# Performance work log

Hardware: AMD Instinct MI355X
Metric: run time of the kernel (lower is better)

The kernel has to match this reference:

```python
import jax, jax.numpy as jnp
import numpy as np

NU, NV = 8192, 8192
IN_DIM, HID, NCLS = 128, 64, 5


def setup_inputs() -> dict:
    key = jax.random.key(0)
    k1, k2, k3, k4, k5, k6, k7 = jax.random.split(key, 7)
    return {
        "u": jax.random.normal(k1, (NU, IN_DIM), dtype=jnp.float32),
        "v": jax.random.normal(k2, (NV, IN_DIM), dtype=jnp.float32),
        "adj": jax.random.uniform(k3, (NU, NV), dtype=jnp.float32),
        "degree": jax.random.uniform(k4, (NU + NV,), dtype=jnp.float32),
        "u_weight": jax.random.normal(k5, (NCLS, IN_DIM, HID), dtype=jnp.float32),
        "v_weight": jax.random.normal(k6, (NCLS, IN_DIM, HID), dtype=jnp.float32),
        "bias": jax.random.normal(k7, (HID,), dtype=jnp.float32),
        "r": 4,
    }


def reference(u, v, adj, degree, u_weight, v_weight, bias, r):
    # Sum weight slices for rating classes 0..r (r is a static Python int).
    Wu = jnp.sum(u_weight[: r + 1], axis=0)  # [IN_DIM, HID]
    Wv = jnp.sum(v_weight[: r + 1], axis=0)
    # Dropout is identity at p=0.0 (eval mode).
    su = u @ Wu  # [NU, HID]
    sv = v @ Wv  # [NV, HID]
    nu = adj.shape[0]
    # Block adjacency [[0, A], [A^T, 0]] row-scaled by diag(degree), applied to
    # concat(su, sv) -- computed block-wise, same math without the dense block matrix.
    top = degree[:nu, None] * (adj @ sv)      # [NU, HID]
    bot = degree[nu:, None] * (adj.T @ su)    # [NV, HID]
    return jnp.concatenate([top, bot], axis=0) + bias
```

## Files before the change

### kernel.cpp

```cpp
#include <hip/hip_runtime.h>
#include <stdint.h>


#define HID 64
#define IN_DIM 128
#define NROWS 8192
#define NCLS 5

typedef float f32x4 __attribute__((ext_vector_type(4)));
typedef short s16x8 __attribute__((ext_vector_type(8)));
typedef unsigned short u16;

#define PACK_SIDE 524288

static __device__ __forceinline__ short f2b(float x) {
    unsigned u = __builtin_bit_cast(unsigned, x);
    return (short)((u + 0x7FFFu + ((u >> 16) & 1u)) >> 16);
}

__global__ __launch_bounds__(256, 2) void k_prep(
    const float* __restrict__ u, const float* __restrict__ v,
    const float* __restrict__ uw, const float* __restrict__ vw,
    const int* __restrict__ rp, u16* __restrict__ ws)
{
    __shared__ float W[IN_DIM * HID];
    __shared__ float X[64 * 129];

    const int y = blockIdx.y;
    const float* __restrict__ src  = y ? v  : u;
    const float* __restrict__ wsrc = y ? vw : uw;
    u16* __restrict__ dstP = ws + (size_t)y * PACK_SIDE;
    const int i0 = blockIdx.x * 64;
    const int t = threadIdx.x;
    int r = *rp; if (r > NCLS - 1) r = NCLS - 1; if (r < 0) r = 0;

    for (int idx = t; idx < IN_DIM * HID; idx += 256) {
        float s = 0.f;
        for (int c = 0; c <= r; ++c) s += wsrc[c * (IN_DIM * HID) + idx];
        W[idx] = s;
    }
    #pragma unroll
    for (int qq = 0; qq < 8; ++qq) {
        int idx = t + qq * 256;
        int row = idx >> 5, c4 = idx & 31;
        f32x4 val = *(const f32x4*)&src[(size_t)(i0 + row) * IN_DIM + c4 * 4];
        float* d = &X[row * 129 + c4 * 4];
        d[0] = val[0]; d[1] = val[1]; d[2] = val[2]; d[3] = val[3];
    }
    __syncthreads();

    const int i = t & 63, h0 = (t >> 6) * 16;
    float acc[16];
    #pragma unroll
    for (int k = 0; k < 16; ++k) acc[k] = 0.f;
    for (int c = 0; c < IN_DIM; ++c) {
        float uv = X[i * 129 + c];
        const f32x4* wr = (const f32x4*)&W[c * HID + h0];
        f32x4 w0 = wr[0], w1 = wr[1], w2 = wr[2], w3 = wr[3];
        acc[0]  += uv * w0[0]; acc[1]  += uv * w0[1];
        acc[2]  += uv * w0[2]; acc[3]  += uv * w0[3];
        acc[4]  += uv * w1[0]; acc[5]  += uv * w1[1];
        acc[6]  += uv * w1[2]; acc[7]  += uv * w1[3];
        acc[8]  += uv * w2[0]; acc[9]  += uv * w2[1];
        acc[10] += uv * w2[2]; acc[11] += uv * w2[3];
        acc[12] += uv * w3[0]; acc[13] += uv * w3[1];
        acc[14] += uv * w3[2]; acc[15] += uv * w3[3];
    }
    const int iL = i0 + i;
    u16* __restrict__ dp = dstP
        + (((size_t)(iL >> 5) * 4 + (h0 >> 4)) << 9)
        + ((iL >> 3) & 3) * 128
        + (iL & 7);
    #pragma unroll
    for (int hh = 0; hh < 16; ++hh)
        dp[hh * 8] = (u16)f2b(acc[hh]);
}

__global__ __launch_bounds__(256, 2) void k_main(
    const float* __restrict__ adj, const float* __restrict__ degree,
    const float* __restrict__ bias, const u16* __restrict__ ws,
    float* __restrict__ out)
{
    __shared__ float S[4][64 * 33];

    const int mode = blockIdx.y;
    const int bx = blockIdx.x;
    const int t = threadIdx.x;
    const int w = t >> 6, l = t & 63;
    const int q = l >> 4, l15 = l & 15;
    const int m0 = bx * 32;
    const unsigned a = (unsigned)(bx >> 1);
    const int kbase = w * 2048;
    const u16* __restrict__ BP = ws + (mode == 0 ? (size_t)PACK_SIDE : 0);
    const u16* __restrict__ BPl = BP + (size_t)l * 8;

    f32x4 acc[2][4];
    #pragma unroll
    for (int i = 0; i < 2; ++i)
        #pragma unroll
        for (int j = 0; j < 4; ++j) acc[i][j] = (f32x4){0.f, 0.f, 0.f, 0.f};

    if (mode == 0) {
        const float* __restrict__ ap0 = adj + (size_t)(m0 + l15) * NROWS;
        const float* __restrict__ ap1 = ap0 + (size_t)16 * NROWS;
        for (int tau = 0; tau < 32; ++tau) {
            const int k0 = kbase + (int)(((a + tau) & 31u) << 6);
            #pragma unroll
            for (int kh = 0; kh < 2; ++kh) {
                const int k = k0 + kh * 32 + q * 8;
                const int kb = (k0 >> 5) + kh;
                f32x4 a00 = *(const f32x4*)(ap0 + k);
                f32x4 a01 = *(const f32x4*)(ap0 + k + 4);
                f32x4 a10 = *(const f32x4*)(ap1 + k);
                f32x4 a11 = *(const f32x4*)(ap1 + k + 4);
                s16x8 bf[4];
                #pragma unroll
                for (int nn = 0; nn < 4; ++nn)
                    bf[nn] = *(const s16x8*)(BPl + ((size_t)(kb * 4 + nn) << 9));
                s16x8 af0, af1;
                af0[0]=f2b(a00[0]); af0[1]=f2b(a00[1]); af0[2]=f2b(a00[2]); af0[3]=f2b(a00[3]);
                af0[4]=f2b(a01[0]); af0[5]=f2b(a01[1]); af0[6]=f2b(a01[2]); af0[7]=f2b(a01[3]);
                af1[0]=f2b(a10[0]); af1[1]=f2b(a10[1]); af1[2]=f2b(a10[2]); af1[3]=f2b(a10[3]);
                af1[4]=f2b(a11[0]); af1[5]=f2b(a11[1]); af1[6]=f2b(a11[2]); af1[7]=f2b(a11[3]);
                #pragma unroll
                for (int nn = 0; nn < 4; ++nn) {
                    acc[0][nn] = __builtin_amdgcn_mfma_f32_16x16x32_bf16(af0, bf[nn], acc[0][nn], 0, 0, 0);
                    acc[1][nn] = __builtin_amdgcn_mfma_f32_16x16x32_bf16(af1, bf[nn], acc[1][nn], 0, 0, 0);
                }
            }
        }
    } else {
        float* __restrict__ T = S[w];
        const int wr_r = l >> 3;
        const int wr_c = (l & 7) * 4;
        const float* __restrict__ cb = adj + m0 + wr_c;
        for (int tau = 0; tau < 32; ++tau) {
            const int i0 = kbase + (int)(((a - tau) & 31u) << 6);
            f32x4 tr[8];
            #pragma unroll
            for (int c = 0; c < 8; ++c)
                tr[c] = *(const f32x4*)(cb + (size_t)(i0 + c * 8 + wr_r) * NROWS);
            #pragma unroll
            for (int c = 0; c < 8; ++c) {
                float* d = &T[(c * 8 + wr_r) * 33 + wr_c];
                d[0] = tr[c][0]; d[1] = tr[c][1]; d[2] = tr[c][2]; d[3] = tr[c][3];
            }
            asm volatile("s_waitcnt lgkmcnt(0)" ::: "memory");
            #pragma unroll
            for (int kh = 0; kh < 2; ++kh) {
                const int kb = (i0 >> 5) + kh;
                s16x8 bf[4];
                #pragma unroll
                for (int nn = 0; nn < 4; ++nn)
                    bf[nn] = *(const s16x8*)(BPl + ((size_t)(kb * 4 + nn) << 9));
                s16x8 af[2];
                #pragma unroll
                for (int mt = 0; mt < 2; ++mt) {
                    const int j = mt * 16 + l15;
                    #pragma unroll
                    for (int tt = 0; tt < 8; ++tt)
                        af[mt][tt] = f2b(T[(kh * 32 + q * 8 + tt) * 33 + j]);
                }
                #pragma unroll
                for (int nn = 0; nn < 4; ++nn) {
                    acc[0][nn] = __builtin_amdgcn_mfma_f32_16x16x32_bf16(af[0], bf[nn], acc[0][nn], 0, 0, 0);
                    acc[1][nn] = __builtin_amdgcn_mfma_f32_16x16x32_bf16(af[1], bf[nn], acc[1][nn], 0, 0, 0);
                }
            }
            asm volatile("" ::: "memory");
        }
    }

    asm volatile("" ::: "memory");
    {
        float* __restrict__ P = S[w];
        #pragma unroll
        for (int mt = 0; mt < 2; ++mt)
            #pragma unroll
            for (int nn = 0; nn < 4; ++nn)
                #pragma unroll
                for (int rg = 0; rg < 4; ++rg)
                    P[(mt * 16 + q * 4 + rg) * 64 + nn * 16 + l15] = acc[mt][nn][rg];
    }
    __syncthreads();

    const int e0 = t * 8;
    const int m = e0 >> 6, n = e0 & 63;
    f32x4 s0 = (f32x4){0.f,0.f,0.f,0.f}, s1 = s0;
    #pragma unroll
    for (int ww = 0; ww < 4; ++ww) {
        s0 += *(const f32x4*)&S[ww][e0];
        s1 += *(const f32x4*)&S[ww][e0 + 4];
    }
    const int grow = (mode ? NROWS : 0) + m0 + m;
    const float d = degree[grow];
    f32x4 b0 = *(const f32x4*)&bias[n];
    f32x4 b1 = *(const f32x4*)&bias[n + 4];
    f32x4 o0 = d * s0 + b0;
    f32x4 o1 = d * s1 + b1;
    *(f32x4*)&out[(size_t)grow * HID + n]     = o0;
    *(f32x4*)&out[(size_t)grow * HID + n + 4] = o1;
}

extern "C" void kernel_launch(void* const* d_in, const int* in_sizes, int n_in,
                              void* d_out, int out_size, void* d_ws, size_t ws_size,
                              hipStream_t stream) {
    (void)in_sizes; (void)n_in; (void)out_size; (void)ws_size;
    const float* u      = (const float*)d_in[0];
    const float* v      = (const float*)d_in[1];
    const float* adj    = (const float*)d_in[2];
    const float* degree = (const float*)d_in[3];
    const float* uw     = (const float*)d_in[4];
    const float* vw     = (const float*)d_in[5];
    const float* bias   = (const float*)d_in[6];
    const int*   rp     = (const int*)d_in[7];
    u16*   ws  = (u16*)d_ws;
    float* out = (float*)d_out;

    k_prep<<<dim3(128, 2), 256, 0, stream>>>(u, v, uw, vw, rp, ws);
    k_main<<<dim3(256, 2), 256, 0, stream>>>(adj, degree, bias, ws, out);
}
```

Before: 467.4 us.

## Prefetch next adjacency tile in registers and rebalance mode-0 blocks

Both branches of the main kernel now load the next adjacency tile into registers while the current tile is converted and fed to MFMA, software-pipelining global loads against compute. Mode-0 blocks shrink to 16 rows, giving 512 such blocks, and the grid is flattened to 768 blocks with launch bounds raised to 3 waves per SIMD for more occupancy. The double-buffered registers raise register pressure. Since the adjacency matrix is read twice, halving mode-0 tile height may lower reuse of the packed B operand.

```diff
diff --git a/kernel.cpp b/kernel.cpp
--- a/kernel.cpp
+++ b/kernel.cpp
@@ -76,79 +76,135 @@
         dp[hh * 8] = (u16)f2b(acc[hh]);
 }
 
-__global__ __launch_bounds__(256, 2) void k_main(
+__global__ __launch_bounds__(256, 3) void k_main(
     const float* __restrict__ adj, const float* __restrict__ degree,
     const float* __restrict__ bias, const u16* __restrict__ ws,
     float* __restrict__ out)
 {
     __shared__ float S[4][64 * 33];
 
-    const int mode = blockIdx.y;
-    const int bx = blockIdx.x;
+    const int bxr = blockIdx.x;
+    const int mode = (bxr >= 512);
     const int t = threadIdx.x;
     const int w = t >> 6, l = t & 63;
     const int q = l >> 4, l15 = l & 15;
-    const int m0 = bx * 32;
-    const unsigned a = (unsigned)(bx >> 1);
     const int kbase = w * 2048;
     const u16* __restrict__ BP = ws + (mode == 0 ? (size_t)PACK_SIDE : 0);
     const u16* __restrict__ BPl = BP + (size_t)l * 8;
 
-    f32x4 acc[2][4];
-    #pragma unroll
-    for (int i = 0; i < 2; ++i)
-        #pragma unroll
-        for (int j = 0; j < 4; ++j) acc[i][j] = (f32x4){0.f, 0.f, 0.f, 0.f};
-
     if (mode == 0) {
-        const float* __restrict__ ap0 = adj + (size_t)(m0 + l15) * NROWS;
-        const float* __restrict__ ap1 = ap0 + (size_t)16 * NROWS;
-        for (int tau = 0; tau < 32; ++tau) {
-            const int k0 = kbase + (int)(((a + tau) & 31u) << 6);
-            #pragma unroll
-            for (int kh = 0; kh < 2; ++kh) {
-                const int k = k0 + kh * 32 + q * 8;
-                const int kb = (k0 >> 5) + kh;
-                f32x4 a00 = *(const f32x4*)(ap0 + k);
-                f32x4 a01 = *(const f32x4*)(ap0 + k + 4);
-                f32x4 a10 = *(const f32x4*)(ap1 + k);
-                f32x4 a11 = *(const f32x4*)(ap1 + k + 4);
-                s16x8 bf[4];
-                #pragma unroll
-                for (int nn = 0; nn < 4; ++nn)
-                    bf[nn] = *(const s16x8*)(BPl + ((size_t)(kb * 4 + nn) << 9));
-                s16x8 af0, af1;
-                af0[0]=f2b(a00[0]); af0[1]=f2b(a00[1]); af0[2]=f2b(a00[2]); af0[3]=f2b(a00[3]);
-                af0[4]=f2b(a01[0]); af0[5]=f2b(a01[1]); af0[6]=f2b(a01[2]); af0[7]=f2b(a01[3]);
-                af1[0]=f2b(a10[0]); af1[1]=f2b(a10[1]); af1[2]=f2b(a10[2]); af1[3]=f2b(a10[3]);
-                af1[4]=f2b(a11[0]); af1[5]=f2b(a11[1]); af1[6]=f2b(a11[2]); af1[7]=f2b(a11[3]);
-                #pragma unroll
-                for (int nn = 0; nn < 4; ++nn) {
-                    acc[0][nn] = __builtin_amdgcn_mfma_f32_16x16x32_bf16(af0, bf[nn], acc[0][nn], 0, 0, 0);
-                    acc[1][nn] = __builtin_amdgcn_mfma_f32_16x16x32_bf16(af1, bf[nn], acc[1][nn], 0, 0, 0);
+        const int bx = bxr;
+        const int m0 = bx * 16;
+        const unsigned a = (unsigned)(bx >> 2);
+        const float* __restrict__ ap0 = adj + (size_t)(m0 + l15) * NROWS + q * 8;
+
+        f32x4 acc[4];
+        #pragma unroll
+        for (int nn = 0; nn < 4; ++nn) acc[nn] = (f32x4){0.f, 0.f, 0.f, 0.f};
+
+        {
+            const int k0 = kbase + (int)((a & 31u) << 6);
+            f32x4 c00 = *(const f32x4*)(ap0 + k0);
+            f32x4 c01 = *(const f32x4*)(ap0 + k0 + 4);
+            f32x4 c10 = *(const f32x4*)(ap0 + k0 + 32);
+            f32x4 c11 = *(const f32x4*)(ap0 + k0 + 36);
+            for (int tau = 0; tau < 32; ++tau) {
+                const int k0c = kbase + (int)(((a + tau) & 31u) << 6);
+                const int tnx = (tau < 31) ? tau + 1 : tau;
+                const int k0n = kbase + (int)(((a + tnx) & 31u) << 6);
+                f32x4 n00 = *(const f32x4*)(ap0 + k0n);
+                f32x4 n01 = *(const f32x4*)(ap0 + k0n + 4);
+                f32x4 n10 = *(const f32x4*)(ap0 + k0n + 32);
+                f32x4 n11 = *(const f32x4*)(ap0 + k0n + 36);
+
+                #pragma unroll
+                for (int kh = 0; kh < 2; ++kh) {
+                    const int kb = (k0c >> 5) + kh;
+                    s16x8 bf[4];
+                    #pragma unroll
+                    for (int nn = 0; nn < 4; ++nn)
+                        bf[nn] = *(const s16x8*)(BPl + ((size_t)(kb * 4 + nn) << 9));
+                    s16x8 af;
+                    if (kh == 0) {
+                        af[0]=f2b(c00[0]); af[1]=f2b(c00[1]); af[2]=f2b(c00[2]); af[3]=f2b(c00[3]);
+                        af[4]=f2b(c01[0]); af[5]=f2b(c01[1]); af[6]=f2b(c01[2]); af[7]=f2b(c01[3]);
+                    } else {
+                        af[0]=f2b(c10[0]); af[1]=f2b(c10[1]); af[2]=f2b(c10[2]); af[3]=f2b(c10[3]);
+                        af[4]=f2b(c11[0]); af[5]=f2b(c11[1]); af[6]=f2b(c11[2]); af[7]=f2b(c11[3]);
+                    }
+                    #pragma unroll
+                    for (int nn = 0; nn < 4; ++nn)
+                        acc[nn] = __builtin_amdgcn_mfma_f32_16x16x32_bf16(af, bf[nn], acc[nn], 0, 0, 0);
                 }
+                c00 = n00; c01 = n01; c10 = n10; c11 = n11;
             }
         }
-    } else {
+
+        asm volatile("" ::: "memory");
+        {
+            float* __restrict__ P = S[w];
+            #pragma unroll
+            for (int nn = 0; nn < 4; ++nn)
+                #pragma unroll
+                for (int rg = 0; rg < 4; ++rg)
+                    P[(q * 4 + rg) * 64 + nn * 16 + l15] = acc[nn][rg];
+        }
+        __syncthreads();
+
+        const int e0 = t * 4;
+        const int m = e0 >> 6, n = e0 & 63;
+        f32x4 s = (f32x4){0.f, 0.f, 0.f, 0.f};
+        #pragma unroll
+        for (int ww = 0; ww < 4; ++ww) s += *(const f32x4*)&S[ww][e0];
+        const int grow = m0 + m;
+        const float d = degree[grow];
+        f32x4 b = *(const f32x4*)&bias[n];
+        *(f32x4*)&out[(size_t)grow * HID + n] = d * s + b;
+        return;
+    }
+
+    {
+        const int bx = bxr - 512;
+        const int m0 = bx * 32;
+        const unsigned a = (unsigned)(bx >> 1);
         float* __restrict__ T = S[w];
         const int wr_r = l >> 3;
         const int wr_c = (l & 7) * 4;
         const float* __restrict__ cb = adj + m0 + wr_c;
-        for (int tau = 0; tau < 32; ++tau) {
-            const int i0 = kbase + (int)(((a - tau) & 31u) << 6);
-            f32x4 tr[8];
+
+        f32x4 acc[2][4];
+        #pragma unroll
+        for (int i = 0; i < 2; ++i)
+            #pragma unroll
+            for (int j = 0; j < 4; ++j) acc[i][j] = (f32x4){0.f, 0.f, 0.f, 0.f};
+
+        f32x4 tr[8];
+        {
+            const int i0 = kbase + (int)((a & 31u) << 6);
             #pragma unroll
             for (int c = 0; c < 8; ++c)
                 tr[c] = *(const f32x4*)(cb + (size_t)(i0 + c * 8 + wr_r) * NROWS);
+        }
+        for (int tau = 0; tau < 32; ++tau) {
+            const int i0c = kbase + (int)(((a - tau) & 31u) << 6);
+            const int tnx = (tau < 31) ? tau + 1 : tau;
+            const int i0n = kbase + (int)(((a - tnx) & 31u) << 6);
+
             #pragma unroll
             for (int c = 0; c < 8; ++c) {
                 float* d = &T[(c * 8 + wr_r) * 33 + wr_c];
                 d[0] = tr[c][0]; d[1] = tr[c][1]; d[2] = tr[c][2]; d[3] = tr[c][3];
             }
             asm volatile("s_waitcnt lgkmcnt(0)" ::: "memory");
+
+            f32x4 trn[8];
+            #pragma unroll
+            for (int c = 0; c < 8; ++c)
+                trn[c] = *(const f32x4*)(cb + (size_t)(i0n + c * 8 + wr_r) * NROWS);
+
             #pragma unroll
             for (int kh = 0; kh < 2; ++kh) {
-                const int kb = (i0 >> 5) + kh;
+                const int kb = (i0c >> 5) + kh;
                 s16x8 bf[4];
                 #pragma unroll
                 for (int nn = 0; nn < 4; ++nn)
@@ -168,38 +224,38 @@
                 }
             }
             asm volatile("" ::: "memory");
-        }
-    }
-
-    asm volatile("" ::: "memory");
-    {
-        float* __restrict__ P = S[w];
-        #pragma unroll
-        for (int mt = 0; mt < 2; ++mt)
-            #pragma unroll
-            for (int nn = 0; nn < 4; ++nn)
-                #pragma unroll
-                for (int rg = 0; rg < 4; ++rg)
-                    P[(mt * 16 + q * 4 + rg) * 64 + nn * 16 + l15] = acc[mt][nn][rg];
-    }
-    __syncthreads();
-
-    const int e0 = t * 8;
-    const int m = e0 >> 6, n = e0 & 63;
-    f32x4 s0 = (f32x4){0.f,0.f,0.f,0.f}, s1 = s0;
-    #pragma unroll
-    for (int ww = 0; ww < 4; ++ww) {
-        s0 += *(const f32x4*)&S[ww][e0];
-        s1 += *(const f32x4*)&S[ww][e0 + 4];
-    }
-    const int grow = (mode ? NROWS : 0) + m0 + m;
-    const float d = degree[grow];
-    f32x4 b0 = *(const f32x4*)&bias[n];
-    f32x4 b1 = *(const f32x4*)&bias[n + 4];
-    f32x4 o0 = d * s0 + b0;
-    f32x4 o1 = d * s1 + b1;
-    *(f32x4*)&out[(size_t)grow * HID + n]     = o0;
-    *(f32x4*)&out[(size_t)grow * HID + n + 4] = o1;
+            #pragma unroll
+            for (int c = 0; c < 8; ++c) tr[c] = trn[c];
+        }
+
+        asm volatile("" ::: "memory");
+        {
+            float* __restrict__ P = S[w];
+            #pragma unroll
+            for (int mt = 0; mt < 2; ++mt)
+                #pragma unroll
+                for (int nn = 0; nn < 4; ++nn)
+                    #pragma unroll
+                    for (int rg = 0; rg < 4; ++rg)
+                        P[(mt * 16 + q * 4 + rg) * 64 + nn * 16 + l15] = acc[mt][nn][rg];
+        }
+        __syncthreads();
+
+        const int e0 = t * 8;
+        const int m = e0 >> 6, n = e0 & 63;
+        f32x4 s0 = (f32x4){0.f,0.f,0.f,0.f}, s1 = s0;
+        #pragma unroll
+        for (int ww = 0; ww < 4; ++ww) {
+            s0 += *(const f32x4*)&S[ww][e0];
+            s1 += *(const f32x4*)&S[ww][e0 + 4];
+        }
+        const int grow = NROWS + m0 + m;
+        const float d = degree[grow];
+        f32x4 b0 = *(const f32x4*)&bias[n];
+        f32x4 b1 = *(const f32x4*)&bias[n + 4];
+        *(f32x4*)&out[(size_t)grow * HID + n]     = d * s0 + b0;
+        *(f32x4*)&out[(size_t)grow * HID + n + 4] = d * s1 + b1;
+    }
 }
 
 extern "C" void kernel_launch(void* const* d_in, const int* in_sizes, int n_in,
@@ -218,5 +274,5 @@
     float* out = (float*)d_out;
 
     k_prep<<<dim3(128, 2), 256, 0, stream>>>(u, v, uw, vw, rp, ws);
-    k_main<<<dim3(256, 2), 256, 0, stream>>>(adj, degree, bias, ws, out);
-}
+    k_main<<<dim3(768),    256, 0, stream>>>(adj, degree, bias, ws, out);
+}
```

Measured after the change: 489.4 us. 1.05x slower.

## Read adjacency once per 256x256 tile for both products, reduce partials in separate kernel

Applied to the files above, without the earlier changes.

Replaces the two-mode main kernel, which streamed adj once row-wise and once transposed, with a single pass. Each block loads a 256x256 adj tile into swizzled bf16 LDS, and its waves compute both the adj@sv and adj^T@su contributions from that tile. Per-tile partial sums go to large fp32 workspace buffers (32 partials per output row). A new finalize kernel then sums those partials and applies degree and bias. This removes the second adj read and the strided transposed loads, but adds roughly 134MB of partial-sum writes and reads plus an extra launch. It also relies on a much larger workspace, and the transposed side builds its fragments from scalar 16-bit LDS reads.

```diff
diff --git a/kernel.cpp b/kernel.cpp
--- a/kernel.cpp
+++ b/kernel.cpp
@@ -9,6 +9,7 @@
 
 typedef float f32x4 __attribute__((ext_vector_type(4)));
 typedef short s16x8 __attribute__((ext_vector_type(8)));
+typedef short s16x4 __attribute__((ext_vector_type(4)));
 typedef unsigned short u16;
 
 #define PACK_SIDE 524288
@@ -77,129 +78,142 @@
 }
 
 __global__ __launch_bounds__(256, 2) void k_main(
-    const float* __restrict__ adj, const float* __restrict__ degree,
-    const float* __restrict__ bias, const u16* __restrict__ ws,
-    float* __restrict__ out)
+    const float* __restrict__ adj, const u16* __restrict__ ws,
+    float* __restrict__ wst, float* __restrict__ wsb)
 {
-    __shared__ float S[4][64 * 33];
-
-    const int mode = blockIdx.y;
+    __shared__ u16 P[64][256];
+
     const int bx = blockIdx.x;
+    const int R0 = (bx >> 5) * 256, C0 = (bx & 31) * 256;
     const int t = threadIdx.x;
     const int w = t >> 6, l = t & 63;
     const int q = l >> 4, l15 = l & 15;
-    const int m0 = bx * 32;
-    const unsigned a = (unsigned)(bx >> 1);
-    const int kbase = w * 2048;
-    const u16* __restrict__ BP = ws + (mode == 0 ? (size_t)PACK_SIDE : 0);
-    const u16* __restrict__ BPl = BP + (size_t)l * 8;
-
-    f32x4 acc[2][4];
-    #pragma unroll
-    for (int i = 0; i < 2; ++i)
+    const u16* __restrict__ BPl_u = ws + (size_t)l * 8;
+    const u16* __restrict__ BPl_v = ws + PACK_SIDE + (size_t)l * 8;
+
+    f32x4 accB[8][4];
+    #pragma unroll
+    for (int mt = 0; mt < 8; ++mt)
         #pragma unroll
-        for (int j = 0; j < 4; ++j) acc[i][j] = (f32x4){0.f, 0.f, 0.f, 0.f};
-
-    if (mode == 0) {
-        const float* __restrict__ ap0 = adj + (size_t)(m0 + l15) * NROWS;
-        const float* __restrict__ ap1 = ap0 + (size_t)16 * NROWS;
-        for (int tau = 0; tau < 32; ++tau) {
-            const int k0 = kbase + (int)(((a + tau) & 31u) << 6);
-            #pragma unroll
-            for (int kh = 0; kh < 2; ++kh) {
-                const int k = k0 + kh * 32 + q * 8;
-                const int kb = (k0 >> 5) + kh;
-                f32x4 a00 = *(const f32x4*)(ap0 + k);
-                f32x4 a01 = *(const f32x4*)(ap0 + k + 4);
-                f32x4 a10 = *(const f32x4*)(ap1 + k);
-                f32x4 a11 = *(const f32x4*)(ap1 + k + 4);
-                s16x8 bf[4];
-                #pragma unroll
-                for (int nn = 0; nn < 4; ++nn)
-                    bf[nn] = *(const s16x8*)(BPl + ((size_t)(kb * 4 + nn) << 9));
-                s16x8 af0, af1;
-                af0[0]=f2b(a00[0]); af0[1]=f2b(a00[1]); af0[2]=f2b(a00[2]); af0[3]=f2b(a00[3]);
-                af0[4]=f2b(a01[0]); af0[5]=f2b(a01[1]); af0[6]=f2b(a01[2]); af0[7]=f2b(a01[3]);
-                af1[0]=f2b(a10[0]); af1[1]=f2b(a10[1]); af1[2]=f2b(a10[2]); af1[3]=f2b(a10[3]);
-                af1[4]=f2b(a11[0]); af1[5]=f2b(a11[1]); af1[6]=f2b(a11[2]); af1[7]=f2b(a11[3]);
-                #pragma unroll
-                for (int nn = 0; nn < 4; ++nn) {
-                    acc[0][nn] = __builtin_amdgcn_mfma_f32_16x16x32_bf16(af0, bf[nn], acc[0][nn], 0, 0, 0);
-                    acc[1][nn] = __builtin_amdgcn_mfma_f32_16x16x32_bf16(af1, bf[nn], acc[1][nn], 0, 0, 0);
+        for (int nn = 0; nn < 4; ++nn) accB[mt][nn] = (f32x4){0.f, 0.f, 0.f, 0.f};
+
+    for (int p = 0; p < 4; ++p) {
+        {
+            const float* __restrict__ src =
+                adj + (size_t)(R0 + p * 64 + w * 16) * NROWS + C0 + l * 4;
+            #pragma unroll
+            for (int rr = 0; rr < 16; rr += 4) {
+                f32x4 d0 = *(const f32x4*)(src + (size_t)(rr + 0) * NROWS);
+                f32x4 d1 = *(const f32x4*)(src + (size_t)(rr + 1) * NROWS);
+                f32x4 d2 = *(const f32x4*)(src + (size_t)(rr + 2) * NROWS);
+                f32x4 d3 = *(const f32x4*)(src + (size_t)(rr + 3) * NROWS);
+                #pragma unroll
+                for (int i = 0; i < 4; ++i) {
+                    f32x4 d = (i == 0) ? d0 : (i == 1) ? d1 : (i == 2) ? d2 : d3;
+                    const int row = w * 16 + rr + i;
+                    s16x4 b;
+                    b[0] = f2b(d[0]); b[1] = f2b(d[1]);
+                    b[2] = f2b(d[2]); b[3] = f2b(d[3]);
+                    *(s16x4*)&P[row][(((l >> 1) ^ (row & 7)) << 3) + ((l & 1) << 2)] = b;
                 }
             }
         }
-    } else {
-        float* __restrict__ T = S[w];
-        const int wr_r = l >> 3;
-        const int wr_c = (l & 7) * 4;
-        const float* __restrict__ cb = adj + m0 + wr_c;
-        for (int tau = 0; tau < 32; ++tau) {
-            const int i0 = kbase + (int)(((a - tau) & 31u) << 6);
-            f32x4 tr[8];
-            #pragma unroll
-            for (int c = 0; c < 8; ++c)
-                tr[c] = *(const f32x4*)(cb + (size_t)(i0 + c * 8 + wr_r) * NROWS);
-            #pragma unroll
-            for (int c = 0; c < 8; ++c) {
-                float* d = &T[(c * 8 + wr_r) * 33 + wr_c];
-                d[0] = tr[c][0]; d[1] = tr[c][1]; d[2] = tr[c][2]; d[3] = tr[c][3];
-            }
-            asm volatile("s_waitcnt lgkmcnt(0)" ::: "memory");
-            #pragma unroll
-            for (int kh = 0; kh < 2; ++kh) {
-                const int kb = (i0 >> 5) + kh;
+        __syncthreads();
+
+        if (w < 2) {
+            f32x4 accT[2][4];
+            #pragma unroll
+            for (int mt = 0; mt < 2; ++mt)
+                #pragma unroll
+                for (int nn = 0; nn < 4; ++nn) accT[mt][nn] = (f32x4){0.f, 0.f, 0.f, 0.f};
+            #pragma unroll
+            for (int kk = 0; kk < 8; ++kk) {
+                const int kb = (C0 >> 5) + kk;
                 s16x8 bf[4];
                 #pragma unroll
                 for (int nn = 0; nn < 4; ++nn)
-                    bf[nn] = *(const s16x8*)(BPl + ((size_t)(kb * 4 + nn) << 9));
-                s16x8 af[2];
+                    bf[nn] = *(const s16x8*)(BPl_v + ((size_t)(kb * 4 + nn) << 9));
                 #pragma unroll
                 for (int mt = 0; mt < 2; ++mt) {
-                    const int j = mt * 16 + l15;
-                    #pragma unroll
-                    for (int tt = 0; tt < 8; ++tt)
-                        af[mt][tt] = f2b(T[(kh * 32 + q * 8 + tt) * 33 + j]);
-                }
-                #pragma unroll
-                for (int nn = 0; nn < 4; ++nn) {
-                    acc[0][nn] = __builtin_amdgcn_mfma_f32_16x16x32_bf16(af[0], bf[nn], acc[0][nn], 0, 0, 0);
-                    acc[1][nn] = __builtin_amdgcn_mfma_f32_16x16x32_bf16(af[1], bf[nn], acc[1][nn], 0, 0, 0);
+                    const int row = w * 32 + mt * 16 + l15;
+                    s16x8 af = *(const s16x8*)&P[row][((kk * 4 + q) ^ (row & 7)) << 3];
+                    #pragma unroll
+                    for (int nn = 0; nn < 4; ++nn)
+                        accT[mt][nn] = __builtin_amdgcn_mfma_f32_16x16x32_bf16(
+                            af, bf[nn], accT[mt][nn], 0, 0, 0);
                 }
             }
-            asm volatile("" ::: "memory");
+            float* __restrict__ WT = wst + (size_t)(bx & 31) * (NROWS * HID)
+                                   + (size_t)(R0 + p * 64 + w * 32) * HID;
+            #pragma unroll
+            for (int mt = 0; mt < 2; ++mt)
+                #pragma unroll
+                for (int nn = 0; nn < 4; ++nn)
+                    #pragma unroll
+                    for (int rg = 0; rg < 4; ++rg)
+                        WT[(size_t)(mt * 16 + q * 4 + rg) * HID + nn * 16 + l15] =
+                            accT[mt][nn][rg];
+        } else {
+            #pragma unroll
+            for (int kk = 0; kk < 2; ++kk) {
+                const int kb = (R0 >> 5) + p * 2 + kk;
+                s16x8 bf[4];
+                #pragma unroll
+                for (int nn = 0; nn < 4; ++nn)
+                    bf[nn] = *(const s16x8*)(BPl_u + ((size_t)(kb * 4 + nn) << 9));
+                #pragma unroll
+                for (int mt = 0; mt < 8; ++mt) {
+                    const int j = (w - 2) * 128 + mt * 16 + l15;
+                    s16x8 af;
+                    #pragma unroll
+                    for (int tt = 0; tt < 8; ++tt) {
+                        const int row = kk * 32 + q * 8 + tt;
+                        af[tt] = (short)P[row][(((j >> 3) ^ tt) << 3) + (j & 7)];
+                    }
+                    #pragma unroll
+                    for (int nn = 0; nn < 4; ++nn)
+                        accB[mt][nn] = __builtin_amdgcn_mfma_f32_16x16x32_bf16(
+                            af, bf[nn], accB[mt][nn], 0, 0, 0);
+                }
+            }
         }
-    }
-
-    asm volatile("" ::: "memory");
-    {
-        float* __restrict__ P = S[w];
+        __syncthreads();
+    }
+
+    if (w >= 2) {
+        float* __restrict__ WB = wsb + (size_t)(bx >> 5) * (NROWS * HID)
+                               + (size_t)(C0 + (w - 2) * 128) * HID;
         #pragma unroll
-        for (int mt = 0; mt < 2; ++mt)
+        for (int mt = 0; mt < 8; ++mt)
             #pragma unroll
             for (int nn = 0; nn < 4; ++nn)
                 #pragma unroll
                 for (int rg = 0; rg < 4; ++rg)
-                    P[(mt * 16 + q * 4 + rg) * 64 + nn * 16 + l15] = acc[mt][nn][rg];
-    }
-    __syncthreads();
-
-    const int e0 = t * 8;
-    const int m = e0 >> 6, n = e0 & 63;
-    f32x4 s0 = (f32x4){0.f,0.f,0.f,0.f}, s1 = s0;
-    #pragma unroll
-    for (int ww = 0; ww < 4; ++ww) {
-        s0 += *(const f32x4*)&S[ww][e0];
-        s1 += *(const f32x4*)&S[ww][e0 + 4];
-    }
-    const int grow = (mode ? NROWS : 0) + m0 + m;
+                    WB[(size_t)(mt * 16 + q * 4 + rg) * HID + nn * 16 + l15] =
+                        accB[mt][nn][rg];
+    }
+}
+
+__global__ __launch_bounds__(256, 4) void k_fin(
+    const float* __restrict__ degree, const float* __restrict__ bias,
+    const float* __restrict__ wst, const float* __restrict__ wsb,
+    float* __restrict__ out)
+{
+    const int b = blockIdx.x;
+    const int side = (b >= 512);
+    const int t = threadIdx.x;
+    const int r = (b & 511) * 16 + (t >> 4);
+    const int c4 = (t & 15) * 4;
+    const float* __restrict__ W = side ? wsb : wst;
+
+    f32x4 s = (f32x4){0.f, 0.f, 0.f, 0.f};
+    #pragma unroll
+    for (int c = 0; c < 32; ++c)
+        s += *(const f32x4*)&W[(size_t)c * (NROWS * HID) + (size_t)r * HID + c4];
+    const int grow = side * NROWS + r;
     const float d = degree[grow];
-    f32x4 b0 = *(const f32x4*)&bias[n];
-    f32x4 b1 = *(const f32x4*)&bias[n + 4];
-    f32x4 o0 = d * s0 + b0;
-    f32x4 o1 = d * s1 + b1;
-    *(f32x4*)&out[(size_t)grow * HID + n]     = o0;
-    *(f32x4*)&out[(size_t)grow * HID + n + 4] = o1;
+    f32x4 bb = *(const f32x4*)&bias[c4];
+    *(f32x4*)&out[(size_t)grow * HID + c4] = d * s + bb;
 }
 
 extern "C" void kernel_launch(void* const* d_in, const int* in_sizes, int n_in,
@@ -215,8 +229,11 @@
     const float* bias   = (const float*)d_in[6];
     const int*   rp     = (const int*)d_in[7];
     u16*   ws  = (u16*)d_ws;
+    float* wst = (float*)(ws + 2 * PACK_SIDE);
+    float* wsb = wst + (size_t)32 * NROWS * HID;
     float* out = (float*)d_out;
 
     k_prep<<<dim3(128, 2), 256, 0, stream>>>(u, v, uw, vw, rp, ws);
-    k_main<<<dim3(256, 2), 256, 0, stream>>>(adj, degree, bias, ws, out);
-}
+    k_main<<<dim3(1024),   256, 0, stream>>>(adj, ws, wst, wsb);
+    k_fin <<<dim3(1024),   256, 0, stream>>>(degree, bias, wst, wsb, out);
+}
```

Result: slower. 529.8 us (+13.4%).

## Double-buffer adjacency tiles in LDS via async global_load_lds prefetch

Applied to the files above, without the earlier changes.

Both modes of the main kernel now stage adjacency tiles straight into per-wave LDS with global_load_lds. Each wave uses a double buffer, so while it runs the MFMAs on the current tile the next tile is already loading, and vmcnt waits order the two. This aims to hide the global-memory latency that the earlier synchronous load, convert and compute sequence exposed. It also replaces the register-to-LDS transpose copy in the transposed mode. The cost is doubling LDS use per block to about 67KB, which may limit occupancy, and the padded layout adds some risk of LDS bank conflicts.

```diff
diff --git a/kernel.cpp b/kernel.cpp
--- a/kernel.cpp
+++ b/kernel.cpp
@@ -16,6 +16,12 @@
 static __device__ __forceinline__ short f2b(float x) {
     unsigned u = __builtin_bit_cast(unsigned, x);
     return (short)((u + 0x7FFFu + ((u >> 16) & 1u)) >> 16);
+}
+
+static __device__ __forceinline__ void gload16(const float* g, float* lds) {
+    __builtin_amdgcn_global_load_lds(
+        (const __attribute__((address_space(1))) void*)g,
+        (__attribute__((address_space(3))) void*)lds, 16, 0, 0);
 }
 
 __global__ __launch_bounds__(256, 2) void k_prep(
@@ -81,7 +87,7 @@
     const float* __restrict__ bias, const u16* __restrict__ ws,
     float* __restrict__ out)
 {
-    __shared__ float S[4][64 * 33];
+    __shared__ float L[4][2][2112];
 
     const int mode = blockIdx.y;
     const int bx = blockIdx.x;
@@ -93,6 +99,8 @@
     const int kbase = w * 2048;
     const u16* __restrict__ BP = ws + (mode == 0 ? (size_t)PACK_SIDE : 0);
     const u16* __restrict__ BPl = BP + (size_t)l * 8;
+    float* __restrict__ Lw0 = &L[w][0][0];
+    float* __restrict__ Lw1 = &L[w][1][0];
 
     f32x4 acc[2][4];
     #pragma unroll
@@ -101,79 +109,109 @@
         for (int j = 0; j < 4; ++j) acc[i][j] = (f32x4){0.f, 0.f, 0.f, 0.f};
 
     if (mode == 0) {
-        const float* __restrict__ ap0 = adj + (size_t)(m0 + l15) * NROWS;
-        const float* __restrict__ ap1 = ap0 + (size_t)16 * NROWS;
+        const int sr = l >> 4, sc = l & 15;
+        const float* __restrict__ ab = adj + (size_t)m0 * NROWS + sc * 4;
+        {
+            const int k0 = kbase + (int)((a & 31u) << 6);
+            #pragma unroll
+            for (int i = 0; i < 8; ++i)
+                gload16(ab + (size_t)(i * 4 + sr) * NROWS + k0, Lw0 + i * 264);
+        }
+        #pragma unroll 2
         for (int tau = 0; tau < 32; ++tau) {
-            const int k0 = kbase + (int)(((a + tau) & 31u) << 6);
+            const int k0c = kbase + (int)(((a + tau) & 31u) << 6);
+            const int kb0 = k0c >> 5;
+            s16x8 bf0[4], bf1[4];
+            #pragma unroll
+            for (int nn = 0; nn < 4; ++nn)
+                bf0[nn] = *(const s16x8*)(BPl + ((size_t)(kb0 * 4 + nn) << 9));
+            #pragma unroll
+            for (int nn = 0; nn < 4; ++nn)
+                bf1[nn] = *(const s16x8*)(BPl + ((size_t)((kb0 + 1) * 4 + nn) << 9));
+            if (tau < 31) {
+                const int k0n = kbase + (int)(((a + tau + 1) & 31u) << 6);
+                float* Ln = (tau & 1) ? Lw0 : Lw1;
+                #pragma unroll
+                for (int i = 0; i < 8; ++i)
+                    gload16(ab + (size_t)(i * 4 + sr) * NROWS + k0n, Ln + i * 264);
+                asm volatile("s_waitcnt vmcnt(8)" ::: "memory");
+            } else {
+                asm volatile("s_waitcnt vmcnt(0)" ::: "memory");
+            }
+            __builtin_amdgcn_sched_barrier(0);
+            const float* __restrict__ Lb = (tau & 1) ? Lw1 : Lw0;
             #pragma unroll
             for (int kh = 0; kh < 2; ++kh) {
-                const int k = k0 + kh * 32 + q * 8;
-                const int kb = (k0 >> 5) + kh;
-                f32x4 a00 = *(const f32x4*)(ap0 + k);
-                f32x4 a01 = *(const f32x4*)(ap0 + k + 4);
-                f32x4 a10 = *(const f32x4*)(ap1 + k);
-                f32x4 a11 = *(const f32x4*)(ap1 + k + 4);
-                s16x8 bf[4];
-                #pragma unroll
-                for (int nn = 0; nn < 4; ++nn)
-                    bf[nn] = *(const s16x8*)(BPl + ((size_t)(kb * 4 + nn) << 9));
-                s16x8 af0, af1;
-                af0[0]=f2b(a00[0]); af0[1]=f2b(a00[1]); af0[2]=f2b(a00[2]); af0[3]=f2b(a00[3]);
-                af0[4]=f2b(a01[0]); af0[5]=f2b(a01[1]); af0[6]=f2b(a01[2]); af0[7]=f2b(a01[3]);
-                af1[0]=f2b(a10[0]); af1[1]=f2b(a10[1]); af1[2]=f2b(a10[2]); af1[3]=f2b(a10[3]);
-                af1[4]=f2b(a11[0]); af1[5]=f2b(a11[1]); af1[6]=f2b(a11[2]); af1[7]=f2b(a11[3]);
-                #pragma unroll
-                for (int nn = 0; nn < 4; ++nn) {
-                    acc[0][nn] = __builtin_amdgcn_mfma_f32_16x16x32_bf16(af0, bf[nn], acc[0][nn], 0, 0, 0);
-                    acc[1][nn] = __builtin_amdgcn_mfma_f32_16x16x32_bf16(af1, bf[nn], acc[1][nn], 0, 0, 0);
+                #pragma unroll
+                for (int mt = 0; mt < 2; ++mt) {
+                    const int row = mt * 16 + l15;
+                    const int base = (row >> 2) * 264 + (row & 3) * 64 + (kh * 8 + q * 2) * 4;
+                    f32x4 lo = *(const f32x4*)&Lb[base];
+                    f32x4 hi = *(const f32x4*)&Lb[base + 4];
+                    s16x8 af;
+                    af[0]=f2b(lo[0]); af[1]=f2b(lo[1]); af[2]=f2b(lo[2]); af[3]=f2b(lo[3]);
+                    af[4]=f2b(hi[0]); af[5]=f2b(hi[1]); af[6]=f2b(hi[2]); af[7]=f2b(hi[3]);
+                    #pragma unroll
+                    for (int nn = 0; nn < 4; ++nn)
+                        acc[mt][nn] = __builtin_amdgcn_mfma_f32_16x16x32_bf16(
+                            af, kh ? bf1[nn] : bf0[nn], acc[mt][nn], 0, 0, 0);
                 }
             }
         }
     } else {
-        float* __restrict__ T = S[w];
-        const int wr_r = l >> 3;
-        const int wr_c = (l & 7) * 4;
-        const float* __restrict__ cb = adj + m0 + wr_c;
+        const int sr = l >> 3, sc = l & 7;
+        const float* __restrict__ ab = adj + (size_t)sr * NROWS + m0 + sc * 4;
+        {
+            const int i00 = kbase + (int)((a & 31u) << 6);
+            #pragma unroll
+            for (int i = 0; i < 8; ++i)
+                gload16(ab + (size_t)(i00 + i * 8) * NROWS, Lw0 + i * 264);
+        }
+        #pragma unroll 2
         for (int tau = 0; tau < 32; ++tau) {
-            const int i0 = kbase + (int)(((a - tau) & 31u) << 6);
-            f32x4 tr[8];
-            #pragma unroll
-            for (int c = 0; c < 8; ++c)
-                tr[c] = *(const f32x4*)(cb + (size_t)(i0 + c * 8 + wr_r) * NROWS);
-            #pragma unroll
-            for (int c = 0; c < 8; ++c) {
-                float* d = &T[(c * 8 + wr_r) * 33 + wr_c];
-                d[0] = tr[c][0]; d[1] = tr[c][1]; d[2] = tr[c][2]; d[3] = tr[c][3];
-            }
-            asm volatile("s_waitcnt lgkmcnt(0)" ::: "memory");
+            const int i0c = kbase + (int)(((a - tau) & 31u) << 6);
+            const int kb0 = i0c >> 5;
+            s16x8 bf0[4], bf1[4];
+            #pragma unroll
+            for (int nn = 0; nn < 4; ++nn)
+                bf0[nn] = *(const s16x8*)(BPl + ((size_t)(kb0 * 4 + nn) << 9));
+            #pragma unroll
+            for (int nn = 0; nn < 4; ++nn)
+                bf1[nn] = *(const s16x8*)(BPl + ((size_t)((kb0 + 1) * 4 + nn) << 9));
+            if (tau < 31) {
+                const int i0n = kbase + (int)(((a - tau - 1) & 31u) << 6);
+                float* Ln = (tau & 1) ? Lw0 : Lw1;
+                #pragma unroll
+                for (int i = 0; i < 8; ++i)
+                    gload16(ab + (size_t)(i0n + i * 8) * NROWS, Ln + i * 264);
+                asm volatile("s_waitcnt vmcnt(8)" ::: "memory");
+            } else {
+                asm volatile("s_waitcnt vmcnt(0)" ::: "memory");
+            }
+            __builtin_amdgcn_sched_barrier(0);
+            const float* __restrict__ Lb = (tau & 1) ? Lw1 : Lw0;
             #pragma unroll
             for (int kh = 0; kh < 2; ++kh) {
-                const int kb = (i0 >> 5) + kh;
-                s16x8 bf[4];
-                #pragma unroll
-                for (int nn = 0; nn < 4; ++nn)
-                    bf[nn] = *(const s16x8*)(BPl + ((size_t)(kb * 4 + nn) << 9));
-                s16x8 af[2];
                 #pragma unroll
                 for (int mt = 0; mt < 2; ++mt) {
                     const int j = mt * 16 + l15;
+                    const int gbase = (kh * 4 + q) * 264 + j;
+                    s16x8 af;
                     #pragma unroll
                     for (int tt = 0; tt < 8; ++tt)
-                        af[mt][tt] = f2b(T[(kh * 32 + q * 8 + tt) * 33 + j]);
+                        af[tt] = f2b(Lb[gbase + tt * 32]);
+                    #pragma unroll
+                    for (int nn = 0; nn < 4; ++nn)
+                        acc[mt][nn] = __builtin_amdgcn_mfma_f32_16x16x32_bf16(
+                            af, kh ? bf1[nn] : bf0[nn], acc[mt][nn], 0, 0, 0);
                 }
-                #pragma unroll
-                for (int nn = 0; nn < 4; ++nn) {
-                    acc[0][nn] = __builtin_amdgcn_mfma_f32_16x16x32_bf16(af[0], bf[nn], acc[0][nn], 0, 0, 0);
-                    acc[1][nn] = __builtin_amdgcn_mfma_f32_16x16x32_bf16(af[1], bf[nn], acc[1][nn], 0, 0, 0);
-                }
-            }
-            asm volatile("" ::: "memory");
+            }
         }
     }
 
     asm volatile("" ::: "memory");
     {
-        float* __restrict__ P = S[w];
+        float* __restrict__ P = &L[w][0][0];
         #pragma unroll
         for (int mt = 0; mt < 2; ++mt)
             #pragma unroll
@@ -189,8 +227,9 @@
     f32x4 s0 = (f32x4){0.f,0.f,0.f,0.f}, s1 = s0;
     #pragma unroll
     for (int ww = 0; ww < 4; ++ww) {
-        s0 += *(const f32x4*)&S[ww][e0];
-        s1 += *(const f32x4*)&S[ww][e0 + 4];
+        const float* __restrict__ S = &L[ww][0][0];
+        s0 += *(const f32x4*)&S[e0];
+        s1 += *(const f32x4*)&S[e0 + 4];
     }
     const int grow = (mode ? NROWS : 0) + m0 + m;
     const float d = degree[grow];
```

Measured after the change: 465.4 us. No clear change (-0.4%).
